# Performance work log

Hardware: AMD Instinct MI355X
Metric: run time of the kernel (lower is better)

Reference implementation:

```python
import jax, jax.numpy as jnp
import numpy as np

B, C_IN, N, T = 4, 32, 256, 256
C_OUT, K_HOPS, N_SUP, D_NV = 32, 2, 2, 10
C_MID = (K_HOPS * (N_SUP + 1) + 1) * C_OUT  # 224
NEG = jnp.float32(-1e10)


def causal_conv(x, w, b, dilation):
    # x: [B,C,N,T], w: [O,I,1,kw]; left-pad time so output length == T (causal)
    pad = (w.shape[-1] - 1) * dilation
    y = jax.lax.conv_general_dilated(
        x, w, window_strides=(1, 1), padding=[(0, 0), (pad, 0)],
        rhs_dilation=(1, dilation), dimension_numbers=('NCHW', 'OIHW', 'NCHW'))
    return y + b[None, :, None, None]


def gconv_concat(x, adjs, K):
    # K-hop diffusion over each support, concatenated on channel dim
    out = [x]
    for a in adjs:
        x1 = x
        for _ in range(K):
            x1 = jnp.einsum('ncvl,vw->ncwl', x1, a)
            out.append(x1)
    return jnp.concatenate(out, axis=1)


def mlp(h, w, b):
    # 1x1 conv: [B,Cmid,N,T] x [Cout,Cmid,1,1] -> [B,Cout,N,T]
    return jnp.einsum('ncvl,oc->novl', h, w[:, :, 0, 0]) + b[None, :, None, None]


def setup_inputs() -> dict:
    key = jax.random.key(0)
    ks = jax.random.split(key, 24)
    sc = 0.05
    r = lambda k, shape: jax.random.normal(k, shape, dtype=jnp.float32) * sc
    inp = {
        'x': jax.random.normal(ks[0], (B, C_IN, N, T), dtype=jnp.float32),
        'nodevec1': jax.random.normal(ks[1], (N, D_NV), dtype=jnp.float32),
        'nodevec2': jax.random.normal(ks[2], (D_NV, N), dtype=jnp.float32),
        'support0': jax.random.uniform(ks[3], (N, N), dtype=jnp.float32),
        'support1': jax.random.uniform(ks[4], (N, N), dtype=jnp.float32),
        'w_f1': r(ks[5], (C_OUT, C_IN, 1, 2)), 'b_f1': r(ks[6], (C_OUT,)),
        'w_g1': r(ks[7], (C_OUT, C_IN, 1, 2)), 'b_g1': r(ks[8], (C_OUT,)),
        'w_f2': r(ks[9], (C_OUT, C_OUT, 1, 2)), 'b_f2': r(ks[10], (C_OUT,)),
        'w_g2': r(ks[11], (C_OUT, C_OUT, 1, 2)), 'b_g2': r(ks[12], (C_OUT,)),
        'w_m1': r(ks[13], (C_OUT, C_MID, 1, 1)), 'b_m1': r(ks[14], (C_OUT,)),
        'w_m2': r(ks[15], (C_OUT, C_MID, 1, 1)), 'b_m2': r(ks[16], (C_OUT,)),
    }
    return inp


def reference(x, nodevec1, nodevec2, support0, support1,
              w_f1, b_f1, w_g1, b_g1, w_f2, b_f2, w_g2, b_g2,
              w_m1, b_m1, w_m2, b_m2):
    # adaptive adjacency: relu(mm) with zeros masked to -1e10, row softmax
    a = jax.nn.relu(nodevec1 @ nodevec2)
    adp = jax.nn.softmax(jnp.where(a == 0, NEG, a), axis=1)
    adjs = [support0, support1, adp]

    # block 1: dilated(1) causal gated conv + K-hop diffusion + 1x1 conv
    h = causal_conv(x, w_f1, b_f1, 1) * jax.nn.sigmoid(causal_conv(x, w_g1, b_g1, 1))
    h = mlp(gconv_concat(h, adjs, K_HOPS), w_m1, b_m1)

    # block 2: dilated(2) causal gated conv + K-hop diffusion + 1x1 conv
    h = causal_conv(h, w_f2, b_f2, 2) * jax.nn.sigmoid(causal_conv(h, w_g2, b_g2, 2))
    h = mlp(gconv_concat(h, adjs, K_HOPS), w_m2, b_m2)
    return h
```

## Files before the change

kernel.cpp:

```cpp
#include <hip/hip_runtime.h>
#include <hip/hip_bf16.h>
#include <stdint.h>

typedef unsigned short u16;
typedef __attribute__((ext_vector_type(8))) short short8;
typedef __attribute__((ext_vector_type(4))) short short4a;
typedef __attribute__((ext_vector_type(4))) float f32x4;

__device__ __forceinline__ float bf2f(u16 b){ union {unsigned u; float f;} v; v.u = ((unsigned)b)<<16; return v.f; }
__device__ __forceinline__ u16 f2bf(float f){ union {unsigned u; float f;} v; v.f = f; unsigned r = v.u + 0x7FFF + ((v.u>>16)&1); return (u16)(r>>16); }

__global__ __launch_bounds__(256) void k_adp(const float* __restrict__ nv1, const float* __restrict__ nv2,
                                             float* __restrict__ adp){
  int row = blockIdx.x; int j = threadIdx.x;
  float s = 0.f;
  #pragma unroll
  for(int k=0;k<10;k++) s = fmaf(nv1[row*10+k], nv2[k*256+j], s);
  s = s > 0.f ? s : 0.f;
  float val = (s == 0.f) ? -1e10f : s;
  __shared__ float red[256];
  red[j] = val; __syncthreads();
  for(int off=128; off>0; off>>=1){ if(j<off) red[j] = fmaxf(red[j], red[j+off]); __syncthreads(); }
  float mx = red[0]; __syncthreads();
  float e = __expf(val - mx);
  red[j] = e; __syncthreads();
  for(int off=128; off>0; off>>=1){ if(j<off) red[j] += red[j+off]; __syncthreads(); }
  adp[row*256+j] = e / red[0];
}

__global__ __launch_bounds__(256) void k_badj(const float* __restrict__ s0, const float* __restrict__ s1,
                                              const float* __restrict__ adp, u16* __restrict__ badj){
  int s = blockIdx.x >> 8; int w = blockIdx.x & 255; int v = threadIdx.x;
  const float* src = s==0 ? s0 : (s==1 ? s1 : adp);
  badj[(s<<16) + (w<<8) + v] = f2bf(src[v*256 + w]);
}

__global__ __launch_bounds__(256) void k_wprep(const float* __restrict__ wm1, const float* __restrict__ wm2,
                                               const float* __restrict__ wf1, const float* __restrict__ wg1,
                                               const float* __restrict__ wf2, const float* __restrict__ wg2,
                                               u16* __restrict__ whi, u16* __restrict__ wlo,
                                               u16* __restrict__ wcp){
  int idx = blockIdx.x*256 + threadIdx.x;
  if(idx < 14336){
    float w = (idx < 7168) ? wm1[idx] : wm2[idx-7168];
    u16 hh = f2bf(w);
    whi[idx] = hh;
    wlo[idx] = f2bf(w - bf2f(hh));
  } else {
    int e = idx - 14336;
    int blk = e >> 12; int rem = e & 4095;
    int row = rem >> 6; int kk = rem & 63;
    int tap = kk >> 5; int i = kk & 31; int o = row & 31;
    const float* wsrc = blk ? (row<32 ? wf2 : wg2) : (row<32 ? wf1 : wg1);
    float w = wsrc[(o*32+i)*2 + tap];
    u16 hh = f2bf(w);
    wcp[blk*8192 + 0    + rem] = hh;
    wcp[blk*8192 + 4096 + rem] = f2bf(w - bf2f(hh));
  }
}

__global__ __launch_bounds__(256) void k_tin(const float* __restrict__ x, u16* __restrict__ xT){
  int tile = blockIdx.x & 15; int slice = blockIdx.x >> 4;
  int b = slice >> 5, c = slice & 31;
  int tn0 = (tile & 3) * 64;
  int tt0 = (tile >> 2) * 64;
  const float* src = x + (size_t)slice*65536;
  __shared__ float l[64][65];
  int cc = threadIdx.x & 63, r0 = threadIdx.x >> 6;
  #pragma unroll
  for(int k=0;k<16;k++){ int r = r0 + 4*k;
    l[r][cc] = src[(size_t)(tn0 + r)*256 + tt0 + cc];
  }
  __syncthreads();
  #pragma unroll
  for(int k=0;k<16;k++){ int r = r0 + 4*k;
    xT[(((size_t)b*256 + (tt0+r))*32 + c)*256 + tn0 + cc] = f2bf(l[cc][r]);
  }
}

__global__ __launch_bounds__(256) void k_asq(const u16* __restrict__ badj,
                                             const float* __restrict__ s0, const float* __restrict__ s1,
                                             const float* __restrict__ adp, u16* __restrict__ badj2){
  __shared__ __align__(16) u16 lds[16384];
  int tid = threadIdx.x, bid = blockIdx.x;
  int s = bid >> 2, rt = bid & 3;
  int w0 = rt << 6;
  const u16* T = badj + (s<<16);
  const float* S = s==0 ? s0 : (s==1 ? s1 : adp);
  #pragma unroll
  for(int i=0;i<8;i++){
    int off = i*4096 + tid*16;
    int row = off >> 9;
    int P = (off >> 4) & 31;
    int L = (P & 16) | ((P & 15) ^ (row & 15));
    short8 v = *(const short8*)((const char*)T + (size_t)(w0 + row)*512 + L*16);
    *(short8*)((char*)lds + off) = v;
  }
  __syncthreads();
  int lane = tid & 63, wave = tid >> 6;
  int wr = (wave >> 1) << 5, wc = (wave & 1) << 7;
  f32x4 acc[2][8];
  #pragma unroll
  for(int a=0;a<2;a++)
    #pragma unroll
    for(int q=0;q<8;q++) acc[a][q] = {0.f,0.f,0.f,0.f};
  for(int ks=0; ks<8; ks++){
    short8 afr[2], bfr[8];
    #pragma unroll
    for(int mf=0; mf<2; mf++){
      int row = wr + mf*16 + (lane & 15);
      int L = ks*4 + (lane >> 4);
      int P = (L & 16) | ((L & 15) ^ (row & 15));
      afr[mf] = *(const short8*)&lds[row*256 + P*8];
    }
    #pragma unroll
    for(int nf=0; nf<8; nf++){
      int col = wc + nf*16 + (lane & 15);
      const float* src = S + (size_t)col*256 + ks*32 + (lane>>4)*8;
      #pragma unroll
      for(int jj=0;jj<8;jj++) bfr[nf][jj] = (short)f2bf(src[jj]);
    }
    #pragma unroll
    for(int mf=0;mf<2;mf++)
      #pragma unroll
      for(int nf=0;nf<8;nf++)
        acc[mf][nf] = __builtin_amdgcn_mfma_f32_16x16x32_bf16(afr[mf], bfr[nf], acc[mf][nf], 0,0,0);
  }
  u16* D = badj2 + (s<<16) + (size_t)w0*256;
  #pragma unroll
  for(int mf=0;mf<2;mf++)
    #pragma unroll
    for(int nf=0;nf<8;nf++)
      #pragma unroll
      for(int rr=0;rr<4;rr++){
        int row = wr + mf*16 + (lane>>4)*4 + rr;
        int col = wc + nf*16 + (lane&15);
        D[row*256 + col] = f2bf(acc[mf][nf][rr]);
      }
}

__global__ __launch_bounds__(256) void k_pack(const u16* __restrict__ badj, const u16* __restrict__ badj2,
                                              u16* __restrict__ bpack){
  int t = blockIdx.x*256 + threadIdx.x;
  int lane = t & 63; int cg = (t>>6)&15; int ks = (t>>10)&7; int mat = (t>>13)&1; int s = t>>14;
  const u16* src = (mat ? badj2 : badj) + (s<<16) + (cg*16 + (lane&15))*256 + ks*32 + (lane>>4)*8;
  short8 v = *(const short8*)src;
  *(short8*)(bpack + (size_t)t*8) = v;
}

template<int HILO>
__global__ __launch_bounds__(256) void k_cv(const u16* __restrict__ X0, const u16* __restrict__ X1,
                                            const u16* __restrict__ wcp, int blk, int dil,
                                            const float* __restrict__ bfv, const float* __restrict__ bgv,
                                            u16* __restrict__ outh){
  __shared__ __align__(16) u16 pl[(1+HILO)*2*8192];
  const int NPART = 1+HILO;
  int tid = threadIdx.x, bid = blockIdx.x;
  int b = bid >> 8, t = bid & 255;
  size_t base_cur = ((size_t)(b*256 + t))*8192;
  const u16* Xs[2] = {X0, X1};
  #pragma unroll
  for(int part=0; part<NPART; part++){
    #pragma unroll
    for(int tap=0; tap<2; tap++){
      bool valid = (tap==1) || (t >= dil);
      const u16* src = Xs[part] + base_cur - (tap==0 ? (size_t)dil*8192 : 0);
      char* pb = (char*)pl + (tap*NPART + part)*16384;
      #pragma unroll
      for(int it=0; it<4; it++){
        int off = it*4096 + tid*16;
        int c = off >> 9;
        int byte = off & 511;
        short8 v = {0,0,0,0,0,0,0,0};
        if(valid) v = *(const short8*)(src + (off>>1));
        *(short8*)(pb + c*512 + (byte ^ ((c&24)<<2))) = v;
      }
    }
  }
  int lane = tid & 63, wave = tid >> 6;
  const u16* wb = wcp + blk*8192;
  short8 wfr[4][2][2];
  #pragma unroll
  for(int ot=0;ot<4;ot++)
    #pragma unroll
    for(int ks=0;ks<2;ks++)
      #pragma unroll
      for(int p=0;p<2;p++)
        wfr[ot][ks][p] = *(const short8*)(wb + p*4096 + (ot*16 + (lane&15))*64 + ks*32 + (lane>>4)*8);
  __syncthreads();

  f32x4 acc[4][4];
  #pragma unroll
  for(int a=0;a<4;a++)
    #pragma unroll
    for(int q=0;q<4;q++) acc[a][q] = {0.f,0.f,0.f,0.f};
  int nbase = wave << 6;
  #pragma unroll
  for(int nf=0; nf<4; nf++){
    int n = nbase + nf*16 + (lane & 15);
    #pragma unroll
    for(int ks=0; ks<2; ks++){
      short8 xv[NPART];
      #pragma unroll
      for(int p=0;p<NPART;p++){
        char* pb = (char*)pl + (ks*NPART + p)*16384;
        short8 v;
        #pragma unroll
        for(int jj=0;jj<8;jj++){
          int c = ((lane>>4)<<3) + jj;
          v[jj] = *(const short*)(pb + c*512 + ((n*2) ^ ((c&24)<<2)));
        }
        xv[p] = v;
      }
      #pragma unroll
      for(int ot=0; ot<4; ot++){
        acc[ot][nf] = __builtin_amdgcn_mfma_f32_16x16x32_bf16(wfr[ot][ks][0], xv[0], acc[ot][nf], 0,0,0);
        acc[ot][nf] = __builtin_amdgcn_mfma_f32_16x16x32_bf16(wfr[ot][ks][1], xv[0], acc[ot][nf], 0,0,0);
        if(HILO)
          acc[ot][nf] = __builtin_amdgcn_mfma_f32_16x16x32_bf16(wfr[ot][ks][0], xv[HILO], acc[ot][nf], 0,0,0);
      }
    }
  }
  u16* ob = outh + base_cur;
  #pragma unroll
  for(int ot=0; ot<2; ot++)
    #pragma unroll
    for(int nf=0; nf<4; nf++)
      #pragma unroll
      for(int rr=0; rr<4; rr++){
        int o = ot*16 + (lane>>4)*4 + rr;
        int n = nbase + nf*16 + (lane&15);
        float fv = acc[ot][nf][rr] + bfv[o];
        float gv = acc[ot+2][nf][rr] + bgv[o];
        ob[(size_t)o*256 + n] = f2bf(fv / (1.f + __expf(-gv)));
      }
}

#define LB(KS,FC) (*(const short8*)(bp + ((((KS)*16) + cg0 + (FC))<<9) + (lane<<3)))
#define MF(A,B,C) __builtin_amdgcn_mfma_f32_16x16x32_bf16((A),(B),(C),0,0,0)
#define AF(MFI,KS) (*(const short8*)&lA[(MFI*16 + nlo)*256 + (((KS*4+khi)&16)|(((KS*4+khi)&15)^((MFI*16+nlo)&15)))*8])
template<int MODE>
__global__ __launch_bounds__(256, 5) void k_fuse(const u16* __restrict__ X,
                                                 const u16* __restrict__ bpack,
                                                 const u16* __restrict__ WH, const u16* __restrict__ WL,
                                                 const float* __restrict__ bm,
                                                 float* __restrict__ m, u16* __restrict__ mbh, u16* __restrict__ mbl){
  __shared__ __align__(16) u16 lA[8192];
  __shared__ __align__(16) char lYT[9216];
  int tid = threadIdx.x, bid = blockIdx.x;
  int ch = bid & 1;
  size_t cbase = (size_t)(bid >> 1) * 8192;
  const char* Xb = (const char*)(X + cbase);
  #pragma unroll
  for(int i=0;i<4;i++){
    int off = i*4096 + tid*16;
    int row = off >> 9;
    int P = (off >> 4) & 31;
    int L = (P & 16) | ((P & 15) ^ (row & 15));
    short8 v = *(const short8*)(Xb + (size_t)row*512 + L*16);
    *(short8*)((char*)lA + off) = v;
  }
  __syncthreads();
  int lane = tid & 63, wave = tid >> 6;
  int nlo = lane & 15, khi = lane >> 4;
  int cg0 = ch*8 + wave*2;
  char* myY = lYT + wave*2304;

  f32x4 out00={0,0,0,0}, out01=out00, out10=out00, out11=out00;

  {
    int wiA = nlo*224 + khi*8;
    short8 wh0 = *(const short8*)(WH + wiA);
    short8 wl0 = *(const short8*)(WL + wiA);
    short8 wh1 = *(const short8*)(WH + wiA + 3584);
    short8 wl1 = *(const short8*)(WL + wiA + 3584);
    #pragma unroll
    for(int nf=0;nf<2;nf++){
      int n = (ch*8 + wave*2 + nf)*16 + nlo;
      short8 f; int Lc = n >> 3; int bb = (n & 7)*2;
      #pragma unroll
      for(int j=0;j<8;j++){
        int c = khi*8 + j;
        int P = (Lc & 16) | ((Lc & 15) ^ (c & 15));
        f[j] = *(const u16*)((const char*)lA + c*512 + P*16 + bb);
      }
      if(nf==0){ out00=MF(wh0,f,out00); out00=MF(wl0,f,out00); out10=MF(wh1,f,out10); out10=MF(wl1,f,out10); }
      else     { out01=MF(wh0,f,out01); out01=MF(wl0,f,out01); out11=MF(wh1,f,out11); out11=MF(wl1,f,out11); }
    }
  }

  #pragma unroll
  for(int v=0; v<6; v++){
    const u16* bp = bpack + ((size_t)v << 16);
    f32x4 h00={0,0,0,0}, h01=h00, h10=h00, h11=h00;
    short8 p0 = LB(0,0), p1 = LB(0,1);
    short8 q0 = LB(1,0), q1 = LB(1,1);
    #pragma unroll
    for(int ks=0; ks<8; ks++){
      short8 r0, r1;
      if(ks < 6){ r0 = LB(ks+2,0); r1 = LB(ks+2,1); }
      short8 a0 = AF(0,ks), a1 = AF(1,ks);
      h00 = MF(a0, p0, h00);
      h01 = MF(a0, p1, h01);
      h10 = MF(a1, p0, h10);
      h11 = MF(a1, p1, h11);
      p0 = q0; p1 = q1;
      if(ks < 6){ q0 = r0; q1 = r1; }
    }
    #pragma unroll
    for(int mf=0;mf<2;mf++)
      #pragma unroll
      for(int nf=0;nf<2;nf++){
        f32x4 hv = mf==0 ? (nf==0?h00:h01) : (nf==0?h10:h11);
        short4a wv;
        wv[0] = (short)f2bf(hv[0]); wv[1] = (short)f2bf(hv[1]);
        wv[2] = (short)f2bf(hv[2]); wv[3] = (short)f2bf(hv[3]);
        *(short4a*)(myY + (nf*16+nlo)*72 + mf*32 + khi*8) = wv;
      }
    {
      int wiA = nlo*224 + (v+1)*32 + khi*8;
      short8 wh0 = *(const short8*)(WH + wiA);
      short8 wl0 = *(const short8*)(WL + wiA);
      short8 wh1 = *(const short8*)(WH + wiA + 3584);
      short8 wl1 = *(const short8*)(WL + wiA + 3584);
      #pragma unroll
      for(int nf=0;nf<2;nf++){
        const char* rp = myY + (nf*16+nlo)*72 + khi*16;
        short4a flo = *(const short4a*)rp;
        short4a fhi = *(const short4a*)(rp + 8);
        short8 f = {flo[0],flo[1],flo[2],flo[3],fhi[0],fhi[1],fhi[2],fhi[3]};
        if(nf==0){ out00=MF(wh0,f,out00); out00=MF(wl0,f,out00); out10=MF(wh1,f,out10); out10=MF(wl1,f,out10); }
        else     { out01=MF(wh0,f,out01); out01=MF(wl0,f,out01); out11=MF(wh1,f,out11); out11=MF(wl1,f,out11); }
      }
    }
  }

  #pragma unroll
  for(int ot=0;ot<2;ot++)
    #pragma unroll
    for(int nf=0;nf<2;nf++)
      #pragma unroll
      for(int rr=0;rr<4;rr++){
        f32x4 ov = ot==0 ? (nf==0?out00:out01) : (nf==0?out10:out11);
        int o = ot*16 + khi*4 + rr;
        int n = (ch*8 + wave*2 + nf)*16 + nlo;
        float val = ov[rr] + bm[o];
        size_t a = cbase + (size_t)o*256 + n;
        if(MODE==0){
          u16 hh = f2bf(val);
          mbh[a] = hh;
          mbl[a] = f2bf(val - bf2f(hh));
        } else {
          m[a] = val;
        }
      }
}
#undef LB
#undef MF
#undef AF

__global__ __launch_bounds__(256) void k_tip(const float* __restrict__ m, float* __restrict__ dst){
  int tile = blockIdx.x & 15; int slice = blockIdx.x >> 4;
  int b = slice >> 5, o = slice & 31;
  int tn0 = (tile & 3) * 64, tt0 = (tile >> 2) * 64;
  __shared__ float l[64][65];
  int cc = threadIdx.x & 63, r0 = threadIdx.x >> 6;
  #pragma unroll
  for(int k=0;k<16;k++){ int r = r0 + 4*k;
    l[r][cc] = m[(((size_t)b*256 + (tt0+r))*32 + o)*256 + tn0 + cc];
  }
  __syncthreads();
  #pragma unroll
  for(int k=0;k<16;k++){ int r = r0 + 4*k;
    dst[(((size_t)b*32 + o)*256 + (tn0+r))*256 + tt0 + cc] = l[cc][r];
  }
}

extern "C" void kernel_launch(void* const* d_in, const int* in_sizes, int n_in,
                              void* d_out, int out_size, void* d_ws, size_t ws_size,
                              hipStream_t stream){
  (void)in_sizes; (void)n_in; (void)out_size;
  const float* x    = (const float*)d_in[0];
  const float* nv1  = (const float*)d_in[1];
  const float* nv2  = (const float*)d_in[2];
  const float* sup0 = (const float*)d_in[3];
  const float* sup1 = (const float*)d_in[4];
  const float* wf1 = (const float*)d_in[5];  const float* bf1v = (const float*)d_in[6];
  const float* wg1 = (const float*)d_in[7];  const float* bg1v = (const float*)d_in[8];
  const float* wf2 = (const float*)d_in[9];  const float* bf2v = (const float*)d_in[10];
  const float* wg2 = (const float*)d_in[11]; const float* bg2v = (const float*)d_in[12];
  const float* wm1 = (const float*)d_in[13]; const float* bm1 = (const float*)d_in[14];
  const float* wm2 = (const float*)d_in[15]; const float* bm2 = (const float*)d_in[16];
  float* out = (float*)d_out;
  char* ws = (char*)d_ws;
  const size_t MB = (size_t)1 << 20;

  u16*  badj  = (u16*)ws;
  u16*  badj2 = (u16*)(ws + 393216);
  float* adp  = (float*)(ws + 786432);
  u16*  whi   = (u16*)(ws + 1048576);
  u16*  wlo   = (u16*)(ws + 1077248);
  u16*  wcp   = (u16*)(ws + 1105920);
  u16*  bpack = (u16*)(ws + 1179648);

  int tier = (ws_size >= 100*MB) ? 0 : 1;
  u16* h   = (u16*)(ws + 2*MB);
  u16* mbh = (u16*)(ws + 18*MB);
  u16* mbl = (u16*)(ws + 34*MB);
  u16* xT;
  float *m, *tmp = nullptr;
  if(tier==0){
    m  = (float*)(ws + 50*MB);
    xT = (u16*)(ws + 82*MB);
  } else {
    xT = mbh;
    m  = out;
    tmp = (float*)(ws + 2*MB);
  }

  k_adp<<<256,256,0,stream>>>(nv1, nv2, adp);
  k_badj<<<768,256,0,stream>>>(sup0, sup1, adp, badj);
  k_wprep<<<88,256,0,stream>>>(wm1, wm2, wf1, wg1, wf2, wg2, whi, wlo, wcp);
  k_asq<<<12,256,0,stream>>>(badj, sup0, sup1, adp, badj2);
  k_pack<<<192,256,0,stream>>>(badj, badj2, bpack);
  k_tin<<<2048,256,0,stream>>>(x, xT);

  k_cv<0><<<1024,256,0,stream>>>(xT, (const u16*)0, wcp, 0, 1, bf1v, bg1v, h);
  k_fuse<0><<<2048,256,0,stream>>>(h, bpack, whi, wlo, bm1, (float*)0, mbh, mbl);
  k_cv<1><<<1024,256,0,stream>>>(mbh, mbl, wcp, 1, 2, bf2v, bg2v, h);
  k_fuse<1><<<2048,256,0,stream>>>(h, bpack, whi+7168, wlo+7168, bm2, m, (u16*)0, (u16*)0);

  if(tier==0){
    k_tip<<<2048,256,0,stream>>>(m, out);
  } else {
    k_tip<<<2048,256,0,stream>>>(m, tmp);
    hipMemcpyAsync(out, tmp, (size_t)32*MB, hipMemcpyDeviceToDevice, stream);
  }
}
```

Baseline: 190.8 us.

## Pipeline bpack loads across support steps with rotating triple buffer in k_fuse

Replaces the per-support prefetch of bpack fragments, which restarted at each of the six outer iterations, with a continuous 48-step rotating three-slot register pipeline that prefetches across support boundaries. Wraps MFMA groups in s_setprio to favour matrix issue, and uses v_cvt_pk_bf16_f32 for packed float-to-bf16 conversion. Lowers the launch-bounds occupancy hint from 5 to 4 to allow more registers for the deeper prefetch. The aim is to hide global load latency at the start of each support; the cost is fewer resident waves. The packed conversion's rounding may differ slightly from the manual f2bf routine.

```diff
diff --git a/kernel.cpp b/kernel.cpp
--- a/kernel.cpp
+++ b/kernel.cpp
@@ -5,6 +5,7 @@
 typedef unsigned short u16;
 typedef __attribute__((ext_vector_type(8))) short short8;
 typedef __attribute__((ext_vector_type(4))) short short4a;
+typedef __attribute__((ext_vector_type(2))) unsigned int u32x2;
 typedef __attribute__((ext_vector_type(4))) float f32x4;
 
 __device__ __forceinline__ float bf2f(u16 b){ union {unsigned u; float f;} v; v.u = ((unsigned)b)<<16; return v.f; }
@@ -236,11 +237,11 @@
       }
 }
 
-#define LB(KS,FC) (*(const short8*)(bp + ((((KS)*16) + cg0 + (FC))<<9) + (lane<<3)))
+#define LBF(V,KS,FC) (*(const short8*)(bpack + ((size_t)(V)<<16) + ((((KS)*16) + cg0 + (FC))<<9) + (lane<<3)))
 #define MF(A,B,C) __builtin_amdgcn_mfma_f32_16x16x32_bf16((A),(B),(C),0,0,0)
 #define AF(MFI,KS) (*(const short8*)&lA[(MFI*16 + nlo)*256 + (((KS*4+khi)&16)|(((KS*4+khi)&15)^((MFI*16+nlo)&15)))*8])
 template<int MODE>
-__global__ __launch_bounds__(256, 5) void k_fuse(const u16* __restrict__ X,
+__global__ __launch_bounds__(256, 4) void k_fuse(const u16* __restrict__ X,
                                                  const u16* __restrict__ bpack,
                                                  const u16* __restrict__ WH, const u16* __restrict__ WL,
                                                  const float* __restrict__ bm,
@@ -268,6 +269,10 @@
 
   f32x4 out00={0,0,0,0}, out01=out00, out10=out00, out11=out00;
 
+  short8 pA = LBF(0,0,0), pB = LBF(0,0,1);
+  short8 qA = LBF(0,1,0), qB = LBF(0,1,1);
+  short8 rA = LBF(0,2,0), rB = LBF(0,2,1);
+
   {
     int wiA = nlo*224 + khi*8;
     short8 wh0 = *(const short8*)(WH + wiA);
@@ -291,31 +296,36 @@
 
   #pragma unroll
   for(int v=0; v<6; v++){
-    const u16* bp = bpack + ((size_t)v << 16);
     f32x4 h00={0,0,0,0}, h01=h00, h10=h00, h11=h00;
-    short8 p0 = LB(0,0), p1 = LB(0,1);
-    short8 q0 = LB(1,0), q1 = LB(1,1);
     #pragma unroll
     for(int ks=0; ks<8; ks++){
-      short8 r0, r1;
-      if(ks < 6){ r0 = LB(ks+2,0); r1 = LB(ks+2,1); }
+      const int step = v*8 + ks;
       short8 a0 = AF(0,ks), a1 = AF(1,ks);
-      h00 = MF(a0, p0, h00);
-      h01 = MF(a0, p1, h01);
-      h10 = MF(a1, p0, h10);
-      h11 = MF(a1, p1, h11);
-      p0 = q0; p1 = q1;
-      if(ks < 6){ q0 = r0; q1 = r1; }
+      __builtin_amdgcn_s_setprio(1);
+      if(step%3==0){
+        h00=MF(a0,pA,h00); h01=MF(a0,pB,h01); h10=MF(a1,pA,h10); h11=MF(a1,pB,h11);
+      } else if(step%3==1){
+        h00=MF(a0,qA,h00); h01=MF(a0,qB,h01); h10=MF(a1,qA,h10); h11=MF(a1,qB,h11);
+      } else {
+        h00=MF(a0,rA,h00); h01=MF(a0,rB,h01); h10=MF(a1,rA,h10); h11=MF(a1,rB,h11);
+      }
+      __builtin_amdgcn_s_setprio(0);
+      if(step+3 < 48){
+        const int s2 = step+3, V2 = s2>>3, K2 = s2&7;
+        if(step%3==0){ pA = LBF(V2,K2,0); pB = LBF(V2,K2,1); }
+        else if(step%3==1){ qA = LBF(V2,K2,0); qB = LBF(V2,K2,1); }
+        else { rA = LBF(V2,K2,0); rB = LBF(V2,K2,1); }
+      }
     }
     #pragma unroll
     for(int mf=0;mf<2;mf++)
       #pragma unroll
       for(int nf=0;nf<2;nf++){
         f32x4 hv = mf==0 ? (nf==0?h00:h01) : (nf==0?h10:h11);
-        short4a wv;
-        wv[0] = (short)f2bf(hv[0]); wv[1] = (short)f2bf(hv[1]);
-        wv[2] = (short)f2bf(hv[2]); wv[3] = (short)f2bf(hv[3]);
-        *(short4a*)(myY + (nf*16+nlo)*72 + mf*32 + khi*8) = wv;
+        u32x2 wv;
+        asm("v_cvt_pk_bf16_f32 %0, %1, %2" : "=v"(wv[0]) : "v"(hv[0]), "v"(hv[1]));
+        asm("v_cvt_pk_bf16_f32 %0, %1, %2" : "=v"(wv[1]) : "v"(hv[2]), "v"(hv[3]));
+        *(u32x2*)(myY + (nf*16+nlo)*72 + mf*32 + khi*8) = wv;
       }
     {
       int wiA = nlo*224 + (v+1)*32 + khi*8;
@@ -323,6 +333,7 @@
       short8 wl0 = *(const short8*)(WL + wiA);
       short8 wh1 = *(const short8*)(WH + wiA + 3584);
       short8 wl1 = *(const short8*)(WL + wiA + 3584);
+      __builtin_amdgcn_s_setprio(1);
       #pragma unroll
       for(int nf=0;nf<2;nf++){
         const char* rp = myY + (nf*16+nlo)*72 + khi*16;
@@ -332,6 +343,7 @@
         if(nf==0){ out00=MF(wh0,f,out00); out00=MF(wl0,f,out00); out10=MF(wh1,f,out10); out10=MF(wl1,f,out10); }
         else     { out01=MF(wh0,f,out01); out01=MF(wl0,f,out01); out11=MF(wh1,f,out11); out11=MF(wl1,f,out11); }
       }
+      __builtin_amdgcn_s_setprio(0);
     }
   }
 
@@ -355,7 +367,7 @@
         }
       }
 }
-#undef LB
+#undef LBF
 #undef MF
 #undef AF
 
```

Result: no change. 190.2 us (-0.3%).

## Process two time slices per block in k_fuse to reuse adjacency fragments

Applied to the files above, without the earlier changes.

Each k_fuse block now loads two (b,t) slices into double LDS buffers and computes both with one pass over the packed adjacency fragments, halving the grid. Adjacency fragment loads are shared across slices and software-pipelined four steps ahead across support boundaries. This cuts global reads of bpack per unit of work, at the cost of doubled LDS, more registers and lower occupancy (launch bounds drop to 3 waves per SIMD).

```diff
diff --git a/kernel.cpp b/kernel.cpp
--- a/kernel.cpp
+++ b/kernel.cpp
@@ -236,37 +236,78 @@
       }
 }
 
-#define LB(KS,FC) (*(const short8*)(bp + ((((KS)*16) + cg0 + (FC))<<9) + (lane<<3)))
+__device__ __forceinline__ short8 gathA(const u16* TB, int n, int khi){
+  short8 f; int Lc = n >> 3; int bb = (n & 7)*2;
+  #pragma unroll
+  for(int j=0;j<8;j++){
+    int c = khi*8 + j;
+    int P = (Lc & 16) | ((Lc & 15) ^ (c & 15));
+    f[j] = (short)*(const u16*)((const char*)TB + c*512 + P*16 + bb);
+  }
+  return f;
+}
+__device__ __forceinline__ short8 gathY(const char* myY, int nl, int khi){
+  const char* rp = myY + nl*72 + khi*16;
+  short4a g0 = *(const short4a*)rp;
+  short4a g1 = *(const short4a*)(rp + 8);
+  return (short8){g0[0],g0[1],g0[2],g0[3],g1[0],g1[1],g1[2],g1[3]};
+}
+
+#define LBP(BASE,K2,FC) (*(const short8*)((BASE) + (((K2)*16 + cg0 + (FC))<<9) + (lane<<3)))
 #define MF(A,B,C) __builtin_amdgcn_mfma_f32_16x16x32_bf16((A),(B),(C),0,0,0)
-#define AF(MFI,KS) (*(const short8*)&lA[(MFI*16 + nlo)*256 + (((KS*4+khi)&16)|(((KS*4+khi)&15)^((MFI*16+nlo)&15)))*8])
+#define AFU(U,MFI,KS) (*(const short8*)&lA[U][((MFI)*16 + nlo)*256 + ((((KS)*4+khi)&16)|((((KS)*4+khi)&15)^(((MFI)*16+nlo)&15)))*8])
+#define STEP(KS,BA,BB) \
+  { short8 a00=AFU(0,0,KS), a01=AFU(0,1,KS), a10=AFU(1,0,KS), a11=AFU(1,1,KS); \
+    hA00=MF(a00,BA,hA00); hA01=MF(a00,BB,hA01); hA10=MF(a01,BA,hA10); hA11=MF(a01,BB,hA11); \
+    hB00=MF(a10,BA,hB00); hB01=MF(a10,BB,hB01); hB10=MF(a11,BA,hB10); hB11=MF(a11,BB,hB11); \
+    if((KS)<4 || v<5){ const u16* nb = ((KS)<4 ? bpv : bpn); \
+      BA = LBP(nb,((KS)+4)&7,0); BB = LBP(nb,((KS)+4)&7,1); } }
+#define MIXU(F0,F1,O00,O01,O10,O11) \
+  { short8 f0=(F0), f1=(F1); \
+    O00=MF(wh0,f0,O00); O00=MF(wl0,f0,O00); O10=MF(wh1,f0,O10); O10=MF(wl1,f0,O10); \
+    O01=MF(wh0,f1,O01); O01=MF(wl0,f1,O01); O11=MF(wh1,f1,O11); O11=MF(wl1,f1,O11); }
 template<int MODE>
-__global__ __launch_bounds__(256, 5) void k_fuse(const u16* __restrict__ X,
+__global__ __launch_bounds__(256, 3) void k_fuse(const u16* __restrict__ X,
                                                  const u16* __restrict__ bpack,
                                                  const u16* __restrict__ WH, const u16* __restrict__ WL,
                                                  const float* __restrict__ bm,
                                                  float* __restrict__ m, u16* __restrict__ mbh, u16* __restrict__ mbl){
-  __shared__ __align__(16) u16 lA[8192];
-  __shared__ __align__(16) char lYT[9216];
+  __shared__ __align__(16) u16 lA[2][8192];
+  __shared__ __align__(16) char lYT[2][9216];
   int tid = threadIdx.x, bid = blockIdx.x;
   int ch = bid & 1;
-  size_t cbase = (size_t)(bid >> 1) * 8192;
-  const char* Xb = (const char*)(X + cbase);
-  #pragma unroll
-  for(int i=0;i<4;i++){
-    int off = i*4096 + tid*16;
-    int row = off >> 9;
-    int P = (off >> 4) & 31;
-    int L = (P & 16) | ((P & 15) ^ (row & 15));
-    short8 v = *(const short8*)(Xb + (size_t)row*512 + L*16);
-    *(short8*)((char*)lA + off) = v;
+  int tp = (bid >> 1) & 127;
+  int b  = bid >> 8;
+  size_t cb0 = ((size_t)b*256 + tp) * 8192;
+  size_t cb1 = cb0 + (size_t)128*8192;
+  #pragma unroll
+  for(int u=0;u<2;u++){
+    const char* Xb = (const char*)(X + (u ? cb1 : cb0));
+    #pragma unroll
+    for(int i=0;i<4;i++){
+      int off = i*4096 + tid*16;
+      int row = off >> 9;
+      int P = (off >> 4) & 31;
+      int L = (P & 16) | ((P & 15) ^ (row & 15));
+      short8 v = *(const short8*)(Xb + (size_t)row*512 + L*16);
+      *(short8*)((char*)&lA[u][0] + off) = v;
+    }
   }
   __syncthreads();
   int lane = tid & 63, wave = tid >> 6;
   int nlo = lane & 15, khi = lane >> 4;
   int cg0 = ch*8 + wave*2;
-  char* myY = lYT + wave*2304;
-
-  f32x4 out00={0,0,0,0}, out01=out00, out10=out00, out11=out00;
+  char* myY0 = &lYT[0][0] + wave*2304;
+  char* myY1 = &lYT[1][0] + wave*2304;
+
+  f32x4 oA00={0,0,0,0}, oA01=oA00, oA10=oA00, oA11=oA00;
+  f32x4 oB00=oA00, oB01=oA00, oB10=oA00, oB11=oA00;
+
+  const u16* bpv = bpack;
+  short8 B0A = LBP(bpv,0,0), B0B = LBP(bpv,0,1);
+  short8 B1A = LBP(bpv,1,0), B1B = LBP(bpv,1,1);
+  short8 B2A = LBP(bpv,2,0), B2B = LBP(bpv,2,1);
+  short8 B3A = LBP(bpv,3,0), B3B = LBP(bpv,3,1);
 
   {
     int wiA = nlo*224 + khi*8;
@@ -274,48 +315,38 @@
     short8 wl0 = *(const short8*)(WL + wiA);
     short8 wh1 = *(const short8*)(WH + wiA + 3584);
     short8 wl1 = *(const short8*)(WL + wiA + 3584);
-    #pragma unroll
-    for(int nf=0;nf<2;nf++){
-      int n = (ch*8 + wave*2 + nf)*16 + nlo;
-      short8 f; int Lc = n >> 3; int bb = (n & 7)*2;
-      #pragma unroll
-      for(int j=0;j<8;j++){
-        int c = khi*8 + j;
-        int P = (Lc & 16) | ((Lc & 15) ^ (c & 15));
-        f[j] = *(const u16*)((const char*)lA + c*512 + P*16 + bb);
-      }
-      if(nf==0){ out00=MF(wh0,f,out00); out00=MF(wl0,f,out00); out10=MF(wh1,f,out10); out10=MF(wl1,f,out10); }
-      else     { out01=MF(wh0,f,out01); out01=MF(wl0,f,out01); out11=MF(wh1,f,out11); out11=MF(wl1,f,out11); }
-    }
-  }
-
-  #pragma unroll
-  for(int v=0; v<6; v++){
-    const u16* bp = bpack + ((size_t)v << 16);
-    f32x4 h00={0,0,0,0}, h01=h00, h10=h00, h11=h00;
-    short8 p0 = LB(0,0), p1 = LB(0,1);
-    short8 q0 = LB(1,0), q1 = LB(1,1);
-    #pragma unroll
-    for(int ks=0; ks<8; ks++){
-      short8 r0, r1;
-      if(ks < 6){ r0 = LB(ks+2,0); r1 = LB(ks+2,1); }
-      short8 a0 = AF(0,ks), a1 = AF(1,ks);
-      h00 = MF(a0, p0, h00);
-      h01 = MF(a0, p1, h01);
-      h10 = MF(a1, p0, h10);
-      h11 = MF(a1, p1, h11);
-      p0 = q0; p1 = q1;
-      if(ks < 6){ q0 = r0; q1 = r1; }
-    }
+    int n0 = (ch*8 + wave*2)*16 + nlo;
+    MIXU(gathA(&lA[0][0], n0, khi), gathA(&lA[0][0], n0+16, khi), oA00, oA01, oA10, oA11);
+    MIXU(gathA(&lA[1][0], n0, khi), gathA(&lA[1][0], n0+16, khi), oB00, oB01, oB10, oB11);
+  }
+
+  #pragma unroll
+  for(int v=0; v<6; ++v){
+    const u16* bpn = bpv + 65536;
+    f32x4 hA00={0,0,0,0}, hA01=hA00, hA10=hA00, hA11=hA00;
+    f32x4 hB00=hA00, hB01=hA00, hB10=hA00, hB11=hA00;
+    STEP(0,B0A,B0B)
+    STEP(1,B1A,B1B)
+    STEP(2,B2A,B2B)
+    STEP(3,B3A,B3B)
+    STEP(4,B0A,B0B)
+    STEP(5,B1A,B1B)
+    STEP(6,B2A,B2B)
+    STEP(7,B3A,B3B)
     #pragma unroll
     for(int mf=0;mf<2;mf++)
       #pragma unroll
       for(int nf=0;nf<2;nf++){
-        f32x4 hv = mf==0 ? (nf==0?h00:h01) : (nf==0?h10:h11);
+        f32x4 hv = mf==0 ? (nf==0?hA00:hA01) : (nf==0?hA10:hA11);
         short4a wv;
-        wv[0] = (short)f2bf(hv[0]); wv[1] = (short)f2bf(hv[1]);
-        wv[2] = (short)f2bf(hv[2]); wv[3] = (short)f2bf(hv[3]);
-        *(short4a*)(myY + (nf*16+nlo)*72 + mf*32 + khi*8) = wv;
+        wv[0]=(short)f2bf(hv[0]); wv[1]=(short)f2bf(hv[1]);
+        wv[2]=(short)f2bf(hv[2]); wv[3]=(short)f2bf(hv[3]);
+        *(short4a*)(myY0 + (nf*16+nlo)*72 + mf*32 + khi*8) = wv;
+        f32x4 gv = mf==0 ? (nf==0?hB00:hB01) : (nf==0?hB10:hB11);
+        short4a xv;
+        xv[0]=(short)f2bf(gv[0]); xv[1]=(short)f2bf(gv[1]);
+        xv[2]=(short)f2bf(gv[2]); xv[3]=(short)f2bf(gv[3]);
+        *(short4a*)(myY1 + (nf*16+nlo)*72 + mf*32 + khi*8) = xv;
       }
     {
       int wiA = nlo*224 + (v+1)*32 + khi*8;
@@ -323,41 +354,42 @@
       short8 wl0 = *(const short8*)(WL + wiA);
       short8 wh1 = *(const short8*)(WH + wiA + 3584);
       short8 wl1 = *(const short8*)(WL + wiA + 3584);
-      #pragma unroll
-      for(int nf=0;nf<2;nf++){
-        const char* rp = myY + (nf*16+nlo)*72 + khi*16;
-        short4a flo = *(const short4a*)rp;
-        short4a fhi = *(const short4a*)(rp + 8);
-        short8 f = {flo[0],flo[1],flo[2],flo[3],fhi[0],fhi[1],fhi[2],fhi[3]};
-        if(nf==0){ out00=MF(wh0,f,out00); out00=MF(wl0,f,out00); out10=MF(wh1,f,out10); out10=MF(wl1,f,out10); }
-        else     { out01=MF(wh0,f,out01); out01=MF(wl0,f,out01); out11=MF(wh1,f,out11); out11=MF(wl1,f,out11); }
-      }
-    }
-  }
-
-  #pragma unroll
-  for(int ot=0;ot<2;ot++)
-    #pragma unroll
-    for(int nf=0;nf<2;nf++)
-      #pragma unroll
-      for(int rr=0;rr<4;rr++){
-        f32x4 ov = ot==0 ? (nf==0?out00:out01) : (nf==0?out10:out11);
-        int o = ot*16 + khi*4 + rr;
-        int n = (ch*8 + wave*2 + nf)*16 + nlo;
-        float val = ov[rr] + bm[o];
-        size_t a = cbase + (size_t)o*256 + n;
-        if(MODE==0){
-          u16 hh = f2bf(val);
-          mbh[a] = hh;
-          mbl[a] = f2bf(val - bf2f(hh));
-        } else {
-          m[a] = val;
+      MIXU(gathY(myY0, nlo, khi), gathY(myY0, 16+nlo, khi), oA00, oA01, oA10, oA11);
+      MIXU(gathY(myY1, nlo, khi), gathY(myY1, 16+nlo, khi), oB00, oB01, oB10, oB11);
+    }
+    bpv = bpn;
+  }
+
+  #pragma unroll
+  for(int u=0;u<2;u++){
+    size_t cb = u ? cb1 : cb0;
+    #pragma unroll
+    for(int ot=0;ot<2;ot++)
+      #pragma unroll
+      for(int nf=0;nf<2;nf++)
+        #pragma unroll
+        for(int rr=0;rr<4;rr++){
+          f32x4 ov = u==0 ? (ot==0 ? (nf==0?oA00:oA01) : (nf==0?oA10:oA11))
+                          : (ot==0 ? (nf==0?oB00:oB01) : (nf==0?oB10:oB11));
+          int o = ot*16 + khi*4 + rr;
+          int n = (ch*8 + wave*2 + nf)*16 + nlo;
+          float val = ov[rr] + bm[o];
+          size_t a = cb + (size_t)o*256 + n;
+          if(MODE==0){
+            u16 hh = f2bf(val);
+            mbh[a] = hh;
+            mbl[a] = f2bf(val - bf2f(hh));
+          } else {
+            m[a] = val;
+          }
         }
-      }
-}
-#undef LB
+  }
+}
+#undef LBP
 #undef MF
-#undef AF
+#undef AFU
+#undef STEP
+#undef MIXU
 
 __global__ __launch_bounds__(256) void k_tip(const float* __restrict__ m, float* __restrict__ dst){
   int tile = blockIdx.x & 15; int slice = blockIdx.x >> 4;
@@ -426,14 +458,14 @@
   k_tin<<<2048,256,0,stream>>>(x, xT);
 
   k_cv<0><<<1024,256,0,stream>>>(xT, (const u16*)0, wcp, 0, 1, bf1v, bg1v, h);
-  k_fuse<0><<<2048,256,0,stream>>>(h, bpack, whi, wlo, bm1, (float*)0, mbh, mbl);
+  k_fuse<0><<<1024,256,0,stream>>>(h, bpack, whi, wlo, bm1, (float*)0, mbh, mbl);
   k_cv<1><<<1024,256,0,stream>>>(mbh, mbl, wcp, 1, 2, bf2v, bg2v, h);
-  k_fuse<1><<<2048,256,0,stream>>>(h, bpack, whi+7168, wlo+7168, bm2, m, (u16*)0, (u16*)0);
+  k_fuse<1><<<1024,256,0,stream>>>(h, bpack, whi+7168, wlo+7168, bm2, m, (u16*)0, (u16*)0);
 
   if(tier==0){
     k_tip<<<2048,256,0,stream>>>(m, out);
   } else {
     k_tip<<<2048,256,0,stream>>>(m, tmp);
-    hipMemcpyAsync(out, tmp, (size_t)32*MB, hipMemcpyDeviceToDevice, stream);
-  }
-}
+    (void)hipMemcpyAsync(out, tmp, (size_t)32*MB, hipMemcpyDeviceToDevice, stream);
+  }
+}
```

New measurement: 461.3 us. 2.42x slower.
